# Performance work log

Hardware: AMD Instinct MI355X
Metric: run time of the kernel (lower is better)

## Reference

```python
import jax, jax.numpy as jnp
import numpy as np

RANK = 8
ALPHA = 8.0 / RANK  # module stores alpha/rank


def setup_inputs() -> dict:
    key = jax.random.key(0)
    k1, k2, k3, k4, k5 = jax.random.split(key, 5)
    M, N = 4096, 4096          # out_features, in_features
    T = 8192                   # flattened batch*seq tokens
    x = jax.random.normal(k1, (T, N), dtype=jnp.float32)
    W = jax.random.normal(k2, (M, N), dtype=jnp.float32) * 0.02
    b = jax.random.normal(k3, (M,), dtype=jnp.float32) * 0.02
    A = jax.random.normal(k4, (M, RANK), dtype=jnp.float32) * 0.01
    B = jax.random.normal(k5, (N, RANK), dtype=jnp.float32) * 0.01
    return {"x": x, "W": W, "b": b, "A": A, "B": B}


def reference(x, W, b, A, B):
    # Faithful to the torch module: delta_W = alpha * (A @ B.T) is materialized
    # [M, N], then out = linear(x) + F.linear(x, delta_W).
    delta_W = ALPHA * (A @ B.T)                 # [M, N]
    return x @ W.T + b + x @ delta_W.T          # [T, M]
```

## Files before the change

### kernel.cpp

```cpp
#include <hip/hip_runtime.h>
#include <cstdint>
#include <cstddef>


#define T_DIM 8192
#define M_DIM 4096
#define N_DIM 4096
#define RANK  8

typedef _Float16 f16x8 __attribute__((ext_vector_type(8)));
typedef float    f32x4 __attribute__((ext_vector_type(4)));

__global__ __launch_bounds__(256)
void cast_x(const float* __restrict__ src, _Float16* __restrict__ dst) {
    size_t i = ((size_t)blockIdx.x * blockDim.x + threadIdx.x) * 8;
    f32x4 v0 = *(const f32x4*)(src + i);
    f32x4 v1 = *(const f32x4*)(src + i + 4);
    f16x8 o;
#pragma unroll
    for (int k = 0; k < 4; ++k) { o[k] = (_Float16)v0[k]; o[4 + k] = (_Float16)v1[k]; }
    *(f16x8*)(dst + i) = o;
}

__global__ __launch_bounds__(256)
void prep_w(const float* __restrict__ W, const float* __restrict__ A,
            const float* __restrict__ B, _Float16* __restrict__ Wh) {
    const size_t c = (size_t)blockIdx.x * 256 + threadIdx.x;
    const int m  = (int)(c >> 9);
    const int n0 = (int)(c & 511) << 3;
    f32x4 a0 = *(const f32x4*)(A + (size_t)m * RANK);
    f32x4 a1 = *(const f32x4*)(A + (size_t)m * RANK + 4);
    const float* wp = W + (size_t)m * N_DIM + n0;
    f32x4 w0 = *(const f32x4*)wp;
    f32x4 w1 = *(const f32x4*)(wp + 4);
    f16x8 o;
#pragma unroll
    for (int k = 0; k < 8; ++k) {
        const float* Bn = B + (size_t)(n0 + k) * RANK;
        f32x4 b0 = *(const f32x4*)Bn;
        f32x4 b1 = *(const f32x4*)(Bn + 4);
        float d = a0[0]*b0[0] + a0[1]*b0[1] + a0[2]*b0[2] + a0[3]*b0[3]
                + a1[0]*b1[0] + a1[1]*b1[1] + a1[2]*b1[2] + a1[3]*b1[3];
        float wv = (k < 4) ? w0[k] : w1[k - 4];
        o[k] = (_Float16)(wv + d);
    }
    *(f16x8*)(Wh + (size_t)m * N_DIM + n0) = o;
}

__device__ static inline void gld16(const _Float16* g, _Float16* l) {
    __builtin_amdgcn_global_load_lds(
        (const __attribute__((address_space(1))) unsigned int*)g,
        (__attribute__((address_space(3))) unsigned int*)l, 16, 0, 0);
}

__global__ __launch_bounds__(512, 2)
void gemm256(const _Float16* __restrict__ Xh, const _Float16* __restrict__ Wh,
             const float* __restrict__ bias, float* __restrict__ out) {
    __shared__ __align__(16) _Float16 lA[2][256 * 64];
    __shared__ __align__(16) _Float16 lB[2][256 * 64];

    const int tid  = threadIdx.x;
    const int lane = tid & 63;
    const int fr   = lane & 15;
    const int fq   = lane >> 4;
    const int w    = tid >> 6;
    const int wr   = w >> 2;
    const int wcn  = w & 3;

    const size_t rowX0 = (size_t)blockIdx.y * 256;
    const size_t rowW0 = (size_t)blockIdx.x * 256;

    const int srow = tid >> 3;
    const int scol = ((tid & 7) * 8) ^ ((srow & 7) * 8);
    const _Float16* sA = Xh + (rowX0 + srow) * N_DIM + scol;
    const _Float16* sBp[4];
#pragma unroll
    for (int cb = 0; cb < 4; ++cb) {
        const int p = cb * 64 + srow;
        const int wrow = ((p >> 5) & 3) * 64 + ((p >> 7) & 1) * 32 + (p & 31);
        sBp[cb] = Wh + (rowW0 + wrow) * N_DIM + scol;
    }

    const int kc0 = (fq * 8) ^ ((fr & 7) * 8);

    f32x4 acc[8][4] = {};
    f16x8 af[4][2], bf[4][2];

#define STAGE_A(b, rb, kt) gld16(sA + (size_t)(rb) * N_DIM + (kt) * 64, \
                                 &lA[b][(rb) * 64 + tid * 8])
#define STAGE_B(b, cb, kt) gld16(sBp[cb] + (size_t)(kt) * 64, \
                                 &lB[b][(cb) * 4096 + tid * 8])

#define LDA(b, qm) do { _Pragma("unroll") \
    for (int ii = 0; ii < 4; ++ii) { \
        const int ro_ = (wr * 128 + (qm) * 64 + ii * 16 + fr) * 64; \
        af[ii][0] = *(const f16x8*)&lA[b][ro_ + kc0]; \
        af[ii][1] = *(const f16x8*)&lA[b][ro_ + (kc0 ^ 32)]; } } while (0)

#define LDB(b, qn) do { _Pragma("unroll") \
    for (int jj = 0; jj < 2; ++jj) { \
        const int ro_ = ((qn) * 128 + wcn * 32 + jj * 16 + fr) * 64; \
        bf[(qn) * 2 + jj][0] = *(const f16x8*)&lB[b][ro_ + kc0]; \
        bf[(qn) * 2 + jj][1] = *(const f16x8*)&lB[b][ro_ + (kc0 ^ 32)]; } } while (0)

#define MMA(qm, qn) do { __builtin_amdgcn_s_setprio(1); \
    _Pragma("unroll") for (int ii = 0; ii < 4; ++ii) \
    _Pragma("unroll") for (int jj = 0; jj < 2; ++jj) { \
        acc[(qm)*4+ii][(qn)*2+jj] = __builtin_amdgcn_mfma_f32_16x16x32_f16( \
            af[ii][0], bf[(qn)*2+jj][0], acc[(qm)*4+ii][(qn)*2+jj], 0, 0, 0); \
        acc[(qm)*4+ii][(qn)*2+jj] = __builtin_amdgcn_mfma_f32_16x16x32_f16( \
            af[ii][1], bf[(qn)*2+jj][1], acc[(qm)*4+ii][(qn)*2+jj], 0, 0, 0); } \
    __builtin_amdgcn_s_setprio(0); \
    __builtin_amdgcn_sched_barrier(0); } while (0)

#define BAR asm volatile("s_barrier" ::: "memory")
#define VW4 asm volatile("s_waitcnt vmcnt(4)" ::: "memory")
#define VW0 asm volatile("s_waitcnt vmcnt(0)" ::: "memory")

    STAGE_A(0, 0, 0);   STAGE_A(0, 128, 0);  STAGE_B(0, 0, 0);  STAGE_B(0, 1, 0);
    STAGE_A(0, 64, 0);  STAGE_A(0, 192, 0);  STAGE_B(0, 2, 0);  STAGE_B(0, 3, 0);
    STAGE_A(1, 0, 1);   STAGE_A(1, 128, 1);  STAGE_B(1, 0, 1);  STAGE_B(1, 1, 1);
    VW4; BAR;

#pragma unroll 1
    for (int n = 0; n < (N_DIM / 128) - 1; ++n) {
        const int ko  = 2 * n + 1;
        const int kne = 2 * n + 2;
        const int kno = 2 * n + 3;
        LDA(0, 0); LDB(0, 0);
        STAGE_A(1, 64, ko); STAGE_A(1, 192, ko); STAGE_B(1, 2, ko); STAGE_B(1, 3, ko);
        BAR; MMA(0, 0); BAR;
        LDB(0, 1);
        BAR; MMA(0, 1); BAR;
        LDA(0, 1); STAGE_A(0, 0, kne); STAGE_A(0, 128, kne);
        BAR; MMA(1, 0); BAR;
        STAGE_B(0, 0, kne); STAGE_B(0, 1, kne);
        BAR; MMA(1, 1); VW4; BAR;
        LDA(1, 0); LDB(1, 0); STAGE_A(0, 64, kne); STAGE_A(0, 192, kne);
        BAR; MMA(0, 0); BAR;
        LDB(1, 1); STAGE_B(0, 2, kne); STAGE_B(0, 3, kne);
        BAR; MMA(0, 1); BAR;
        LDA(1, 1); STAGE_A(1, 0, kno); STAGE_A(1, 128, kno);
        BAR; MMA(1, 0); BAR;
        STAGE_B(1, 0, kno); STAGE_B(1, 1, kno);
        BAR; MMA(1, 1); VW4; BAR;
    }

    {
        const int ko = N_DIM / 64 - 1;
        LDA(0, 0); LDB(0, 0);
        STAGE_A(1, 64, ko); STAGE_A(1, 192, ko); STAGE_B(1, 2, ko); STAGE_B(1, 3, ko);
        BAR; MMA(0, 0); BAR;
        LDB(0, 1);
        BAR; MMA(0, 1); BAR;
        LDA(0, 1);
        BAR; MMA(1, 0); BAR;
        BAR; MMA(1, 1); VW0; BAR;
        LDA(1, 0); LDB(1, 0);
        BAR; MMA(0, 0); BAR;
        LDB(1, 1);
        BAR; MMA(0, 1); BAR;
        LDA(1, 1);
        BAR; MMA(1, 0); BAR;
        MMA(1, 1);
    }

    const int crow0 = (int)rowX0 + wr * 128;
    const int ccol0 = (int)rowW0 + wcn * 64;
    float bv[4];
#pragma unroll
    for (int j = 0; j < 4; ++j) bv[j] = bias[ccol0 + j * 16 + fr];
#pragma unroll
    for (int i = 0; i < 8; ++i) {
#pragma unroll
        for (int r = 0; r < 4; ++r) {
            const size_t row = (size_t)(crow0 + i * 16 + fq * 4 + r);
#pragma unroll
            for (int j = 0; j < 4; ++j)
                out[row * M_DIM + ccol0 + j * 16 + fr] = acc[i][j][r] + bv[j];
        }
    }
#undef STAGE_A
#undef STAGE_B
#undef LDA
#undef LDB
#undef MMA
#undef BAR
#undef VW4
#undef VW0
}

extern "C" void kernel_launch(void* const* d_in, const int* in_sizes, int n_in,
                              void* d_out, int out_size, void* d_ws, size_t ws_size,
                              hipStream_t stream) {
    const float* x = (const float*)d_in[0];
    const float* W = (const float*)d_in[1];
    const float* b = (const float*)d_in[2];
    const float* A = (const float*)d_in[3];
    const float* B = (const float*)d_in[4];
    float* out = (float*)d_out;

    _Float16* Wh = (_Float16*)d_ws;
    _Float16* Xh = (_Float16*)((char*)d_ws + (size_t)M_DIM * N_DIM * 2);

    cast_x<<<((size_t)T_DIM * N_DIM / 8) / 256, 256, 0, stream>>>(x, Xh);
    prep_w<<<((size_t)M_DIM * N_DIM / 8) / 256, 256, 0, stream>>>(W, A, B, Wh);

    dim3 grid(M_DIM / 256, T_DIM / 256);
    gemm256<<<grid, dim3(512, 1, 1), 0, stream>>>(Xh, Wh, b, out);
}
```

Measured before the change: 562.8 us.

## Switch GEMM to 32x32x16 MFMA tiles with coarser two-phase pipeline

Replaces the 16x16x32 f16 MFMA fragments with 32x32x16 MFMAs, so each wave holds 4x2 accumulators of 16 floats and loads K fragments in four 8-element chunks. The main loop is restructured from eight barrier-separated quarter steps per iteration into four larger phases, with fewer barriers and LDS fragment reloads. The larger MFMA shape is meant to raise math throughput per LDS byte read and reduce barrier overhead. The cost is coarser overlap between global staging and compute, plus a different LDS read pattern that may cause bank conflicts.

```diff
diff --git a/kernel.cpp b/kernel.cpp
--- a/kernel.cpp
+++ b/kernel.cpp
@@ -8,8 +8,9 @@
 #define N_DIM 4096
 #define RANK  8
 
-typedef _Float16 f16x8 __attribute__((ext_vector_type(8)));
-typedef float    f32x4 __attribute__((ext_vector_type(4)));
+typedef _Float16 f16x8  __attribute__((ext_vector_type(8)));
+typedef float    f32x4  __attribute__((ext_vector_type(4)));
+typedef float    f32x16 __attribute__((ext_vector_type(16)));
 
 __global__ __launch_bounds__(256)
 void cast_x(const float* __restrict__ src, _Float16* __restrict__ dst) {
@@ -61,8 +62,8 @@
 
     const int tid  = threadIdx.x;
     const int lane = tid & 63;
-    const int fr   = lane & 15;
-    const int fq   = lane >> 4;
+    const int l32  = lane & 31;
+    const int lhi  = lane >> 5;
     const int w    = tid >> 6;
     const int wr   = w >> 2;
     const int wcn  = w & 3;
@@ -81,35 +82,38 @@
         sBp[cb] = Wh + (rowW0 + wrow) * N_DIM + scol;
     }
 
-    const int kc0 = (fq * 8) ^ ((fr & 7) * 8);
+    int rowA[4], rowB[2], chk[4];
+#pragma unroll
+    for (int mb = 0; mb < 4; ++mb) rowA[mb] = (wr * 128 + mb * 32 + l32) * 64;
+#pragma unroll
+    for (int nb = 0; nb < 2; ++nb) rowB[nb] = (nb * 128 + wcn * 32 + l32) * 64;
+#pragma unroll
+    for (int ks = 0; ks < 4; ++ks) chk[ks] = ((ks * 2 + lhi) ^ (lane & 7)) * 8;
 
-    f32x4 acc[8][4] = {};
-    f16x8 af[4][2], bf[4][2];
+    f32x16 acc[4][2] = {};
+    f16x8  af[2][4], bf[2][4];
 
 #define STAGE_A(b, rb, kt) gld16(sA + (size_t)(rb) * N_DIM + (kt) * 64, \
                                  &lA[b][(rb) * 64 + tid * 8])
 #define STAGE_B(b, cb, kt) gld16(sBp[cb] + (size_t)(kt) * 64, \
                                  &lB[b][(cb) * 4096 + tid * 8])
 
-#define LDA(b, qm) do { _Pragma("unroll") \
-    for (int ii = 0; ii < 4; ++ii) { \
-        const int ro_ = (wr * 128 + (qm) * 64 + ii * 16 + fr) * 64; \
-        af[ii][0] = *(const f16x8*)&lA[b][ro_ + kc0]; \
-        af[ii][1] = *(const f16x8*)&lA[b][ro_ + (kc0 ^ 32)]; } } while (0)
+#define LDAF(b, mbase) do { _Pragma("unroll") \
+    for (int mm = 0; mm < 2; ++mm) { _Pragma("unroll") \
+    for (int ks = 0; ks < 4; ++ks) \
+        af[mm][ks] = *(const f16x8*)&lA[b][rowA[(mbase) + mm] + chk[ks]]; } } while (0)
 
-#define LDB(b, qn) do { _Pragma("unroll") \
-    for (int jj = 0; jj < 2; ++jj) { \
-        const int ro_ = ((qn) * 128 + wcn * 32 + jj * 16 + fr) * 64; \
-        bf[(qn) * 2 + jj][0] = *(const f16x8*)&lB[b][ro_ + kc0]; \
-        bf[(qn) * 2 + jj][1] = *(const f16x8*)&lB[b][ro_ + (kc0 ^ 32)]; } } while (0)
+#define LDBF(b) do { _Pragma("unroll") \
+    for (int nb = 0; nb < 2; ++nb) { _Pragma("unroll") \
+    for (int ks = 0; ks < 4; ++ks) \
+        bf[nb][ks] = *(const f16x8*)&lB[b][rowB[nb] + chk[ks]]; } } while (0)
 
-#define MMA(qm, qn) do { __builtin_amdgcn_s_setprio(1); \
-    _Pragma("unroll") for (int ii = 0; ii < 4; ++ii) \
-    _Pragma("unroll") for (int jj = 0; jj < 2; ++jj) { \
-        acc[(qm)*4+ii][(qn)*2+jj] = __builtin_amdgcn_mfma_f32_16x16x32_f16( \
-            af[ii][0], bf[(qn)*2+jj][0], acc[(qm)*4+ii][(qn)*2+jj], 0, 0, 0); \
-        acc[(qm)*4+ii][(qn)*2+jj] = __builtin_amdgcn_mfma_f32_16x16x32_f16( \
-            af[ii][1], bf[(qn)*2+jj][1], acc[(qm)*4+ii][(qn)*2+jj], 0, 0, 0); } \
+#define MMA(mbase) do { __builtin_amdgcn_s_setprio(1); \
+    _Pragma("unroll") for (int mm = 0; mm < 2; ++mm) \
+    _Pragma("unroll") for (int nb = 0; nb < 2; ++nb) \
+    _Pragma("unroll") for (int ks = 0; ks < 4; ++ks) \
+        acc[(mbase) + mm][nb] = __builtin_amdgcn_mfma_f32_32x32x16_f16( \
+            af[mm][ks], bf[nb][ks], acc[(mbase) + mm][nb], 0, 0, 0); \
     __builtin_amdgcn_s_setprio(0); \
     __builtin_amdgcn_sched_barrier(0); } while (0)
 
@@ -117,73 +121,52 @@
 #define VW4 asm volatile("s_waitcnt vmcnt(4)" ::: "memory")
 #define VW0 asm volatile("s_waitcnt vmcnt(0)" ::: "memory")
 
-    STAGE_A(0, 0, 0);   STAGE_A(0, 128, 0);  STAGE_B(0, 0, 0);  STAGE_B(0, 1, 0);
-    STAGE_A(0, 64, 0);  STAGE_A(0, 192, 0);  STAGE_B(0, 2, 0);  STAGE_B(0, 3, 0);
-    STAGE_A(1, 0, 1);   STAGE_A(1, 128, 1);  STAGE_B(1, 0, 1);  STAGE_B(1, 1, 1);
+    STAGE_A(0, 0, 0);  STAGE_A(0, 64, 0);  STAGE_A(0, 128, 0);  STAGE_A(0, 192, 0);
+    STAGE_B(0, 0, 0);  STAGE_B(0, 1, 0);   STAGE_B(0, 2, 0);    STAGE_B(0, 3, 0);
+    STAGE_A(1, 0, 1);  STAGE_A(1, 128, 1); STAGE_B(1, 0, 1);    STAGE_B(1, 1, 1);
     VW4; BAR;
 
 #pragma unroll 1
-    for (int n = 0; n < (N_DIM / 128) - 1; ++n) {
+    for (int n = 0; n < 31; ++n) {
         const int ko  = 2 * n + 1;
-        const int kne = 2 * n + 2;
-        const int kno = 2 * n + 3;
-        LDA(0, 0); LDB(0, 0);
+        const int ke2 = 2 * n + 2;
+        const int ko2 = 2 * n + 3;
         STAGE_A(1, 64, ko); STAGE_A(1, 192, ko); STAGE_B(1, 2, ko); STAGE_B(1, 3, ko);
-        BAR; MMA(0, 0); BAR;
-        LDB(0, 1);
-        BAR; MMA(0, 1); BAR;
-        LDA(0, 1); STAGE_A(0, 0, kne); STAGE_A(0, 128, kne);
-        BAR; MMA(1, 0); BAR;
-        STAGE_B(0, 0, kne); STAGE_B(0, 1, kne);
-        BAR; MMA(1, 1); VW4; BAR;
-        LDA(1, 0); LDB(1, 0); STAGE_A(0, 64, kne); STAGE_A(0, 192, kne);
-        BAR; MMA(0, 0); BAR;
-        LDB(1, 1); STAGE_B(0, 2, kne); STAGE_B(0, 3, kne);
-        BAR; MMA(0, 1); BAR;
-        LDA(1, 1); STAGE_A(1, 0, kno); STAGE_A(1, 128, kno);
-        BAR; MMA(1, 0); BAR;
-        STAGE_B(1, 0, kno); STAGE_B(1, 1, kno);
-        BAR; MMA(1, 1); VW4; BAR;
+        LDBF(0); LDAF(0, 0); MMA(0); BAR;
+        STAGE_A(0, 0, ke2); STAGE_A(0, 128, ke2); STAGE_B(0, 0, ke2); STAGE_B(0, 1, ke2);
+        LDAF(0, 2); MMA(2); VW4; BAR;
+        STAGE_A(0, 64, ke2); STAGE_A(0, 192, ke2); STAGE_B(0, 2, ke2); STAGE_B(0, 3, ke2);
+        LDBF(1); LDAF(1, 0); MMA(0); BAR;
+        STAGE_A(1, 0, ko2); STAGE_A(1, 128, ko2); STAGE_B(1, 0, ko2); STAGE_B(1, 1, ko2);
+        LDAF(1, 2); MMA(2); VW4; BAR;
     }
 
-    {
-        const int ko = N_DIM / 64 - 1;
-        LDA(0, 0); LDB(0, 0);
-        STAGE_A(1, 64, ko); STAGE_A(1, 192, ko); STAGE_B(1, 2, ko); STAGE_B(1, 3, ko);
-        BAR; MMA(0, 0); BAR;
-        LDB(0, 1);
-        BAR; MMA(0, 1); BAR;
-        LDA(0, 1);
-        BAR; MMA(1, 0); BAR;
-        BAR; MMA(1, 1); VW0; BAR;
-        LDA(1, 0); LDB(1, 0);
-        BAR; MMA(0, 0); BAR;
-        LDB(1, 1);
-        BAR; MMA(0, 1); BAR;
-        LDA(1, 1);
-        BAR; MMA(1, 0); BAR;
-        MMA(1, 1);
-    }
+    STAGE_A(1, 64, 63); STAGE_A(1, 192, 63); STAGE_B(1, 2, 63); STAGE_B(1, 3, 63);
+    LDBF(0); LDAF(0, 0); MMA(0); BAR;
+    LDAF(0, 2); MMA(2); VW0; BAR;
+    LDBF(1); LDAF(1, 0); MMA(0);
+    LDAF(1, 2); MMA(2);
 
     const int crow0 = (int)rowX0 + wr * 128;
     const int ccol0 = (int)rowW0 + wcn * 64;
-    float bv[4];
+    float bv[2];
 #pragma unroll
-    for (int j = 0; j < 4; ++j) bv[j] = bias[ccol0 + j * 16 + fr];
+    for (int nb = 0; nb < 2; ++nb) bv[nb] = bias[ccol0 + nb * 32 + l32];
 #pragma unroll
-    for (int i = 0; i < 8; ++i) {
+    for (int mb = 0; mb < 4; ++mb) {
 #pragma unroll
-        for (int r = 0; r < 4; ++r) {
-            const size_t row = (size_t)(crow0 + i * 16 + fq * 4 + r);
+        for (int nb = 0; nb < 2; ++nb) {
 #pragma unroll
-            for (int j = 0; j < 4; ++j)
-                out[row * M_DIM + ccol0 + j * 16 + fr] = acc[i][j][r] + bv[j];
+            for (int r = 0; r < 16; ++r) {
+                const size_t row = (size_t)(crow0 + mb * 32 + (r & 3) + 8 * (r >> 2) + 4 * lhi);
+                out[row * M_DIM + ccol0 + nb * 32 + l32] = acc[mb][nb][r] + bv[nb];
+            }
         }
     }
 #undef STAGE_A
 #undef STAGE_B
-#undef LDA
-#undef LDB
+#undef LDAF
+#undef LDBF
 #undef MMA
 #undef BAR
 #undef VW4
```

Result: slower. 603.7 us (+7.3%).

## Merge prep kernels into one launch and coarsen GEMM main-loop barrier schedule

Applied to the files above, without the earlier changes.

Combines the x cast and the W+LoRA fold into a single prep launch split by block index, removing one kernel launch and its tail. The GEMM main loop is reordered so each half-tile issues its LDS fragment loads for two MMA groups, then runs both MMAs between fewer barriers, with global-to-LDS staging moved between the MMA pairs. The intent is to cut barrier count and per-MMA synchronisation overhead. The cost is longer register lifetimes and a greater risk of LDS hazards if the staging order races with the reads.

```diff
diff --git a/kernel.cpp b/kernel.cpp
--- a/kernel.cpp
+++ b/kernel.cpp
@@ -11,40 +11,42 @@
 typedef _Float16 f16x8 __attribute__((ext_vector_type(8)));
 typedef float    f32x4 __attribute__((ext_vector_type(4)));
 
+#define CAST_BLOCKS 16384
 __global__ __launch_bounds__(256)
-void cast_x(const float* __restrict__ src, _Float16* __restrict__ dst) {
-    size_t i = ((size_t)blockIdx.x * blockDim.x + threadIdx.x) * 8;
-    f32x4 v0 = *(const f32x4*)(src + i);
-    f32x4 v1 = *(const f32x4*)(src + i + 4);
-    f16x8 o;
-#pragma unroll
-    for (int k = 0; k < 4; ++k) { o[k] = (_Float16)v0[k]; o[4 + k] = (_Float16)v1[k]; }
-    *(f16x8*)(dst + i) = o;
-}
-
-__global__ __launch_bounds__(256)
-void prep_w(const float* __restrict__ W, const float* __restrict__ A,
-            const float* __restrict__ B, _Float16* __restrict__ Wh) {
-    const size_t c = (size_t)blockIdx.x * 256 + threadIdx.x;
-    const int m  = (int)(c >> 9);
-    const int n0 = (int)(c & 511) << 3;
-    f32x4 a0 = *(const f32x4*)(A + (size_t)m * RANK);
-    f32x4 a1 = *(const f32x4*)(A + (size_t)m * RANK + 4);
-    const float* wp = W + (size_t)m * N_DIM + n0;
-    f32x4 w0 = *(const f32x4*)wp;
-    f32x4 w1 = *(const f32x4*)(wp + 4);
-    f16x8 o;
-#pragma unroll
-    for (int k = 0; k < 8; ++k) {
-        const float* Bn = B + (size_t)(n0 + k) * RANK;
-        f32x4 b0 = *(const f32x4*)Bn;
-        f32x4 b1 = *(const f32x4*)(Bn + 4);
-        float d = a0[0]*b0[0] + a0[1]*b0[1] + a0[2]*b0[2] + a0[3]*b0[3]
-                + a1[0]*b1[0] + a1[1]*b1[1] + a1[2]*b1[2] + a1[3]*b1[3];
-        float wv = (k < 4) ? w0[k] : w1[k - 4];
-        o[k] = (_Float16)(wv + d);
-    }
-    *(f16x8*)(Wh + (size_t)m * N_DIM + n0) = o;
+void prep_all(const float* __restrict__ x, const float* __restrict__ W,
+              const float* __restrict__ A, const float* __restrict__ B,
+              _Float16* __restrict__ Xh, _Float16* __restrict__ Wh) {
+    const int bid = blockIdx.x;
+    if (bid < CAST_BLOCKS) {
+        size_t i = ((size_t)bid * 256 + threadIdx.x) * 8;
+        f32x4 v0 = *(const f32x4*)(x + i);
+        f32x4 v1 = *(const f32x4*)(x + i + 4);
+        f16x8 o;
+#pragma unroll
+        for (int k = 0; k < 4; ++k) { o[k] = (_Float16)v0[k]; o[4 + k] = (_Float16)v1[k]; }
+        *(f16x8*)(Xh + i) = o;
+    } else {
+        const size_t c = (size_t)(bid - CAST_BLOCKS) * 256 + threadIdx.x;
+        const int m  = (int)(c >> 9);
+        const int n0 = (int)(c & 511) << 3;
+        f32x4 a0 = *(const f32x4*)(A + (size_t)m * RANK);
+        f32x4 a1 = *(const f32x4*)(A + (size_t)m * RANK + 4);
+        const float* wp = W + (size_t)m * N_DIM + n0;
+        f32x4 w0 = *(const f32x4*)wp;
+        f32x4 w1 = *(const f32x4*)(wp + 4);
+        f16x8 o;
+#pragma unroll
+        for (int k = 0; k < 8; ++k) {
+            const float* Bn = B + (size_t)(n0 + k) * RANK;
+            f32x4 b0 = *(const f32x4*)Bn;
+            f32x4 b1 = *(const f32x4*)(Bn + 4);
+            float d = a0[0]*b0[0] + a0[1]*b0[1] + a0[2]*b0[2] + a0[3]*b0[3]
+                    + a1[0]*b1[0] + a1[1]*b1[1] + a1[2]*b1[2] + a1[3]*b1[3];
+            float wv = (k < 4) ? w0[k] : w1[k - 4];
+            o[k] = (_Float16)(wv + d);
+        }
+        *(f16x8*)(Wh + (size_t)m * N_DIM + n0) = o;
+    }
 }
 
 __device__ static inline void gld16(const _Float16* g, _Float16* l) {
@@ -117,67 +119,64 @@
 #define VW4 asm volatile("s_waitcnt vmcnt(4)" ::: "memory")
 #define VW0 asm volatile("s_waitcnt vmcnt(0)" ::: "memory")
 
-    STAGE_A(0, 0, 0);   STAGE_A(0, 128, 0);  STAGE_B(0, 0, 0);  STAGE_B(0, 1, 0);
-    STAGE_A(0, 64, 0);  STAGE_A(0, 192, 0);  STAGE_B(0, 2, 0);  STAGE_B(0, 3, 0);
-    STAGE_A(1, 0, 1);   STAGE_A(1, 128, 1);  STAGE_B(1, 0, 1);  STAGE_B(1, 1, 1);
+    STAGE_A(0, 0, 0);  STAGE_A(0, 64, 0);  STAGE_A(0, 128, 0);  STAGE_A(0, 192, 0);
+    STAGE_B(0, 0, 0);  STAGE_B(0, 1, 0);   STAGE_B(0, 2, 0);    STAGE_B(0, 3, 0);
+    STAGE_A(1, 0, 1);  STAGE_A(1, 128, 1); STAGE_B(1, 0, 1);    STAGE_B(1, 1, 1);
     VW4; BAR;
 
 #pragma unroll 1
-    for (int n = 0; n < (N_DIM / 128) - 1; ++n) {
+    for (int n = 0; n < 31; ++n) {
         const int ko  = 2 * n + 1;
-        const int kne = 2 * n + 2;
-        const int kno = 2 * n + 3;
-        LDA(0, 0); LDB(0, 0);
+        const int ke2 = 2 * n + 2;
+        const int ko2 = 2 * n + 3;
         STAGE_A(1, 64, ko); STAGE_A(1, 192, ko); STAGE_B(1, 2, ko); STAGE_B(1, 3, ko);
-        BAR; MMA(0, 0); BAR;
-        LDB(0, 1);
-        BAR; MMA(0, 1); BAR;
-        LDA(0, 1); STAGE_A(0, 0, kne); STAGE_A(0, 128, kne);
-        BAR; MMA(1, 0); BAR;
-        STAGE_B(0, 0, kne); STAGE_B(0, 1, kne);
-        BAR; MMA(1, 1); VW4; BAR;
-        LDA(1, 0); LDB(1, 0); STAGE_A(0, 64, kne); STAGE_A(0, 192, kne);
-        BAR; MMA(0, 0); BAR;
-        LDB(1, 1); STAGE_B(0, 2, kne); STAGE_B(0, 3, kne);
-        BAR; MMA(0, 1); BAR;
-        LDA(1, 1); STAGE_A(1, 0, kno); STAGE_A(1, 128, kno);
-        BAR; MMA(1, 0); BAR;
-        STAGE_B(1, 0, kno); STAGE_B(1, 1, kno);
-        BAR; MMA(1, 1); VW4; BAR;
-    }
-
+        LDA(0, 0); LDB(0, 0); LDB(0, 1);
+        MMA(0, 0); MMA(0, 1);
+        BAR;
+        STAGE_A(0, 0, ke2); STAGE_A(0, 128, ke2); STAGE_B(0, 0, ke2); STAGE_B(0, 1, ke2);
+        LDA(0, 1);
+        MMA(1, 0); MMA(1, 1);
+        VW4; BAR;
+        STAGE_A(0, 64, ke2); STAGE_A(0, 192, ke2); STAGE_B(0, 2, ke2); STAGE_B(0, 3, ke2);
+        LDA(1, 0); LDB(1, 0); LDB(1, 1);
+        MMA(0, 0); MMA(0, 1);
+        BAR;
+        STAGE_A(1, 0, ko2); STAGE_A(1, 128, ko2); STAGE_B(1, 0, ko2); STAGE_B(1, 1, ko2);
+        LDA(1, 1);
+        MMA(1, 0); MMA(1, 1);
+        VW4; BAR;
+    }
+
+    STAGE_A(1, 64, 63); STAGE_A(1, 192, 63); STAGE_B(1, 2, 63); STAGE_B(1, 3, 63);
+    LDA(0, 0); LDB(0, 0); LDB(0, 1);
+    MMA(0, 0); MMA(0, 1);
+    BAR;
+    LDA(0, 1);
+    MMA(1, 0); MMA(1, 1);
+    VW0; BAR;
+    LDA(1, 0); LDB(1, 0); LDB(1, 1);
+    MMA(0, 0); MMA(0, 1);
+    LDA(1, 1);
+    MMA(1, 0); MMA(1, 1);
+
+    const int crow0 = (int)rowX0 + wr * 64;
+    const int ccol0 = (int)rowW0 + wcn * 64;
+    (void)crow0; (void)ccol0;
     {
-        const int ko = N_DIM / 64 - 1;
-        LDA(0, 0); LDB(0, 0);
-        STAGE_A(1, 64, ko); STAGE_A(1, 192, ko); STAGE_B(1, 2, ko); STAGE_B(1, 3, ko);
-        BAR; MMA(0, 0); BAR;
-        LDB(0, 1);
-        BAR; MMA(0, 1); BAR;
-        LDA(0, 1);
-        BAR; MMA(1, 0); BAR;
-        BAR; MMA(1, 1); VW0; BAR;
-        LDA(1, 0); LDB(1, 0);
-        BAR; MMA(0, 0); BAR;
-        LDB(1, 1);
-        BAR; MMA(0, 1); BAR;
-        LDA(1, 1);
-        BAR; MMA(1, 0); BAR;
-        MMA(1, 1);
-    }
-
-    const int crow0 = (int)rowX0 + wr * 128;
-    const int ccol0 = (int)rowW0 + wcn * 64;
-    float bv[4];
-#pragma unroll
-    for (int j = 0; j < 4; ++j) bv[j] = bias[ccol0 + j * 16 + fr];
-#pragma unroll
-    for (int i = 0; i < 8; ++i) {
-#pragma unroll
-        for (int r = 0; r < 4; ++r) {
-            const size_t row = (size_t)(crow0 + i * 16 + fq * 4 + r);
-#pragma unroll
-            for (int j = 0; j < 4; ++j)
-                out[row * M_DIM + ccol0 + j * 16 + fr] = acc[i][j][r] + bv[j];
+        const int crow = (int)rowX0 + wr * 128;
+        const int ccol = (int)rowW0 + wcn * 64;
+        float bv[4];
+#pragma unroll
+        for (int j = 0; j < 4; ++j) bv[j] = bias[ccol + j * 16 + fr];
+#pragma unroll
+        for (int i = 0; i < 8; ++i) {
+#pragma unroll
+            for (int r = 0; r < 4; ++r) {
+                const size_t row = (size_t)(crow + i * 16 + fq * 4 + r);
+#pragma unroll
+                for (int j = 0; j < 4; ++j)
+                    out[row * M_DIM + ccol + j * 16 + fr] = acc[i][j][r] + bv[j];
+            }
         }
     }
 #undef STAGE_A
@@ -203,8 +202,8 @@
     _Float16* Wh = (_Float16*)d_ws;
     _Float16* Xh = (_Float16*)((char*)d_ws + (size_t)M_DIM * N_DIM * 2);
 
-    cast_x<<<((size_t)T_DIM * N_DIM / 8) / 256, 256, 0, stream>>>(x, Xh);
-    prep_w<<<((size_t)M_DIM * N_DIM / 8) / 256, 256, 0, stream>>>(W, A, B, Wh);
+    prep_all<<<CAST_BLOCKS + (M_DIM * N_DIM / 8) / 256, 256, 0, stream>>>(
+        x, W, A, B, Xh, Wh);
 
     dim3 grid(M_DIM / 256, T_DIM / 256);
     gemm256<<<grid, dim3(512, 1, 1), 0, stream>>>(Xh, Wh, b, out);
```

Result: slower. 575.3 us (+2.2%).
